# Optimization experiments

Measured on AMD Instinct MI355X. Metric: run time of the kernel, lower is better.

## Reference

```python
import jax, jax.numpy as jnp
import numpy as np

K_SIZE = 3
STRIDE = 1
DIL = 1
PAD = (K_SIZE - 1) // 2 * DIL          # padding of the deformable conv
OFF_PAD = (K_SIZE - 1) // 2            # padding of the offset conv
KK = K_SIZE * K_SIZE


def setup_inputs() -> dict:
    key = jax.random.key(0)
    k1, k2, k3, k4 = jax.random.split(key, 4)
    B, C, H, W = 4, 256, 64, 64
    O = 256
    x = jax.random.normal(k1, (B, C, H, W), jnp.float32)
    # offset/mask conv params (small so sampled offsets stay in a realistic range)
    w_off = jax.random.normal(k2, (3 * KK, C, K_SIZE, K_SIZE), jnp.float32) * 0.01
    b_off = jax.random.normal(k3, (3 * KK,), jnp.float32) * 0.01
    # deformable conv weight (conv_dcn has bias=False in the source)
    w_dcn = jax.random.normal(k4, (O, C, K_SIZE, K_SIZE), jnp.float32) * (1.0 / np.sqrt(C * KK))
    return {"x": x, "w_off": w_off, "b_off": b_off, "w_dcn": w_dcn}


def _bilinear_sample(x, ys, xs):
    """x: [B,C,H,W]; ys, xs: [B,KK,Ho,Wo] fractional coords. Zero outside bounds.
    Returns [B,C,KK,Ho,Wo]."""
    B, C, H, W = x.shape
    _, K, Ho, Wo = ys.shape
    y0 = jnp.floor(ys)
    x0 = jnp.floor(xs)
    y1, x1 = y0 + 1.0, x0 + 1.0
    wy1 = ys - y0
    wy0 = 1.0 - wy1
    wx1 = xs - x0
    wx0 = 1.0 - wx1
    x_flat = x.reshape(B, C, H * W)

    def gather_term(yi, xi, wt):
        valid = (yi >= 0) & (yi < H) & (xi >= 0) & (xi < W)
        yc = jnp.clip(yi, 0, H - 1).astype(jnp.int32)
        xc = jnp.clip(xi, 0, W - 1).astype(jnp.int32)
        idx = (yc * W + xc).reshape(B, -1)                      # [B, K*Ho*Wo]
        g = jax.vmap(lambda xf, i: xf[:, i])(x_flat, idx)       # [B, C, K*Ho*Wo]
        w = (wt * valid.astype(wt.dtype)).reshape(B, 1, -1)
        return g * w

    out = (gather_term(y0, x0, wy0 * wx0)
           + gather_term(y0, x1, wy0 * wx1)
           + gather_term(y1, x0, wy1 * wx0)
           + gather_term(y1, x1, wy1 * wx1))
    return out.reshape(B, C, K, Ho, Wo)


def _dcn_v2(x, w_off, b_off, w_dcn):
    B, C, H, W = x.shape
    # offset/mask conv (standard conv, padding (k-1)//2)
    om = jax.lax.conv_general_dilated(
        x, w_off, (STRIDE, STRIDE), [(OFF_PAD, OFF_PAD)] * 2,
        dimension_numbers=("NCHW", "OIHW", "NCHW")) + b_off[None, :, None, None]
    offset = om[:, :2 * KK]                 # [B, 2*KK, Ho, Wo] as (dy0,dx0,dy1,dx1,...)
    mask = jax.nn.sigmoid(om[:, 2 * KK:])   # [B, KK, Ho, Wo]
    Ho, Wo = offset.shape[2], offset.shape[3]

    off = offset.reshape(B, KK, 2, Ho, Wo)
    off_y, off_x = off[:, :, 0], off[:, :, 1]

    kh = (jnp.arange(KK) // K_SIZE).astype(jnp.float32)
    kw = (jnp.arange(KK) % K_SIZE).astype(jnp.float32)
    py = (jnp.arange(Ho) * STRIDE - PAD).astype(jnp.float32)
    px = (jnp.arange(Wo) * STRIDE - PAD).astype(jnp.float32)

    ys = py[None, None, :, None] + (kh * DIL)[None, :, None, None] + off_y
    xs = px[None, None, None, :] + (kw * DIL)[None, :, None, None] + off_x

    sampled = _bilinear_sample(x, ys, xs)           # [B,C,KK,Ho,Wo]
    sampled = sampled * mask[:, None]               # modulated (DCNv2)
    w = w_dcn.reshape(w_dcn.shape[0], C, KK)
    return jnp.einsum("bckhw,ock->bohw", sampled, w)


def reference(x, w_off, b_off, w_dcn):
    return _dcn_v2(x, w_off, b_off, w_dcn)
```

## Files before the change

kernel.cpp:

```cpp
#include <hip/hip_runtime.h>

typedef __attribute__((ext_vector_type(8))) short short8;
typedef __attribute__((ext_vector_type(4))) float f32x4;

#define CIN 256
#define OUTC 256
#define HWW 4096
#define IMG_H 64
#define IMG_W 64
#define SROW 264
#define SB __builtin_amdgcn_sched_barrier(0)
#define GLOAD(dst, addr) \
    asm volatile("global_load_dwordx4 %0, %1, off" : "=v"(dst) : "v"(addr) : "memory")
#define WAITVM(n) asm volatile("s_waitcnt vmcnt(" #n ")" ::: "memory")
#define WAITLGKM  asm volatile("s_waitcnt lgkmcnt(0)" ::: "memory")

__device__ __forceinline__ short f2bf(float f) {
    unsigned u = __float_as_uint(f);
    u += 0x7fffu + ((u >> 16) & 1u);
    return (short)(u >> 16);
}
__device__ __forceinline__ float bf2f(short s) {
    return __uint_as_float(((unsigned)(unsigned short)s) << 16);
}

__global__ __launch_bounds__(256) void prep(const float* __restrict__ x,
                                            const float* __restrict__ w_dcn,
                                            const float* __restrict__ w_off,
                                            short* __restrict__ xT,
                                            short* __restrict__ wF,
                                            short* __restrict__ wFo) {
    int bid = blockIdx.x;
    if (bid < 1024) {
        __shared__ float T[64][65];
        int p0 = (bid & 63) * 64;
        int c0 = ((bid >> 6) & 3) * 64;
        int b  = bid >> 8;
        int j = threadIdx.x & 63, i = threadIdx.x >> 6;
        const float* xb = x + ((size_t)b * CIN + c0) * HWW + p0;
#pragma unroll
        for (int k = 0; k < 16; ++k) {
            int row = i * 16 + k;
            T[row][j] = xb[(size_t)row * HWW + j];
        }
        __syncthreads();
        short* xTb = xT + ((size_t)b * HWW + p0) * CIN + c0;
#pragma unroll
        for (int k = 0; k < 16; ++k) {
            int prow = i * 16 + k;
            xTb[(size_t)prow * CIN + j] = f2bf(T[j][prow]);
        }
    } else if (bid < 1312) {
        int g = (bid - 1024) * 256 + threadIdx.x;
        int lane = g & 63;
        int rest = g >> 6;
        int octile = rest & 15;
        int step = rest >> 4;
        int kp = step >> 3, chv = step & 7;
        int oc = octile * 16 + (lane & 15);
        int cbase = chv * 32 + (lane >> 4) * 8;
        short8 v;
#pragma unroll
        for (int j = 0; j < 8; ++j)
            v[j] = f2bf(w_dcn[oc * 2304 + (cbase + j) * 9 + kp]);
        *(short8*)(wF + (size_t)g * 8) = v;
    } else {
        int g = (bid - 1312) * 256 + threadIdx.x;
        int lane = g & 63;
        int rest = g >> 6;
        int octile = rest & 1;
        int step = rest >> 1;
        int kp = step >> 3, chv = step & 7;
        int oc = octile * 16 + (lane & 15);
        int cbase = chv * 32 + (lane >> 4) * 8;
        short8 v;
#pragma unroll
        for (int j = 0; j < 8; ++j)
            v[j] = (oc < 27) ? f2bf(w_off[(oc * 256 + cbase + j) * 9 + kp]) : (short)0;
        *(short8*)(wFo + (size_t)g * 8) = v;
    }
}

__global__ __launch_bounds__(256) void offs_mfma(
        const short* __restrict__ xT, const short* __restrict__ wFo,
        float* __restrict__ P) {
    __shared__ short Sm[2][32 * SROW];

    int tid = threadIdx.x;
    int d = blockIdx.x;
    int L = (d & 7) * 64 + (d >> 3);
    int b = L >> 7;
    int ph = L & 127;
    int pbase = ph * 32;
    int prow = ph >> 1;
    int pc0 = (ph & 1) * 32;
    const short* xTb = xT + (size_t)b * HWW * CIN;

    int lane = tid & 63, wave = tid >> 6;
    int fr = lane & 15, fq = lane >> 4;
    int octile = wave & 1, pxt = wave >> 1;

    short8 st[4];

    auto loads = [&](int kp) {
        int yy = prow - 1 + kp / 3;
        int dx = kp % 3 - 1;
#pragma unroll
        for (int it = 0; it < 4; ++it) {
            int item = tid + it * 256;
            int cg8 = item & 31, px = item >> 5;
            int xx = pc0 + px + dx;
            bool ok = (yy >= 0 && yy < IMG_H && xx >= 0 && xx < IMG_W);
            int idx = ok ? ((yy * IMG_W + xx) * CIN + cg8 * 8) : 0;
            short8 v = *(const short8*)&xTb[idx];
            if (!ok) v = (short8){0,0,0,0,0,0,0,0};
            st[it] = v;
        }
    };
    auto writes = [&](int bufi) {
#pragma unroll
        for (int it = 0; it < 4; ++it) {
            int item = tid + it * 256;
            int cg8 = item & 31, px = item >> 5;
            *(short8*)&Sm[bufi][px * SROW + cg8 * 8] = st[it];
        }
    };

    f32x4 acc = (f32x4){0.f, 0.f, 0.f, 0.f};

    loads(0); writes(0);
    __syncthreads();
    for (int kp = 0; kp < 9; ++kp) {
        short8 aF[8];
#pragma unroll
        for (int chv = 0; chv < 8; ++chv)
            aF[chv] = *(const short8*)(wFo +
                    (((size_t)((kp * 8 + chv) * 2 + octile)) * 64 + lane) * 8);
        if (kp < 8) loads(kp + 1);
        const short* SmB = Sm[kp & 1];
#pragma unroll
        for (int chv = 0; chv < 8; ++chv) {
            short8 bF = *(const short8*)&SmB[(pxt * 16 + fr) * SROW + chv * 32 + fq * 8];
            acc = __builtin_amdgcn_mfma_f32_16x16x32_bf16(aF[chv], bF, acc, 0, 0, 0);
        }
        if (kp < 8) writes((kp + 1) & 1);
        __syncthreads();
    }

#pragma unroll
    for (int r = 0; r < 4; ++r) {
        int oc = octile * 16 + fq * 4 + r;
        if (oc < 27)
            P[((size_t)b * 32 + oc) * HWW + pbase + pxt * 16 + fr] = acc[r];
    }
}

__global__ __launch_bounds__(512, 2) void dcn_main(
        const short* __restrict__ xT, const float* __restrict__ b_off,
        const float* __restrict__ P, const short* __restrict__ wF,
        float* __restrict__ out) {
    __shared__ short Sm[2][16 * 64 * 8];
    __shared__ float4 preW[576];
    __shared__ int4  preI[576];

    int tid = threadIdx.x;
    int d = blockIdx.x;
    int L = (d & 7) * 32 + (d >> 3);
    int b = L >> 6;
    int row = L & 63;
    int pbase = row * 64;
    const short* xTb = xT + (size_t)b * HWW * CIN;

    for (int e = tid; e < 576; e += 512) {
        int px = e & 63, kp = e >> 6;
        int p = pbase + px;
        float oy = P[((size_t)b * 32 + 2 * kp) * HWW + p] + b_off[2 * kp];
        float ox = P[((size_t)b * 32 + 2 * kp + 1) * HWW + p] + b_off[2 * kp + 1];
        float ml = P[((size_t)b * 32 + 18 + kp) * HWW + p] + b_off[18 + kp];
        float m = 1.0f / (1.0f + expf(-ml));
        float ys = (float)(row - 1 + kp / 3) + oy;
        float xs = (float)(px - 1 + kp % 3) + ox;
        float y0f = floorf(ys), x0f = floorf(xs);
        float fy = ys - y0f, fx = xs - x0f;
        int iy0 = (int)y0f, ix0 = (int)x0f;
        int iy1 = iy0 + 1, ix1 = ix0 + 1;
        float vy0 = (iy0 >= 0 && iy0 < IMG_H) ? 1.f : 0.f;
        float vy1 = (iy1 >= 0 && iy1 < IMG_H) ? 1.f : 0.f;
        float vx0 = (ix0 >= 0 && ix0 < IMG_W) ? 1.f : 0.f;
        float vx1 = (ix1 >= 0 && ix1 < IMG_W) ? 1.f : 0.f;
        int ry0 = min(max(iy0, 0), IMG_H - 1) * IMG_W;
        int ry1 = min(max(iy1, 0), IMG_H - 1) * IMG_W;
        int cx0 = min(max(ix0, 0), IMG_W - 1);
        int cx1 = min(max(ix1, 0), IMG_W - 1);
        float wy0 = 1.f - fy, wy1 = fy, wx0 = 1.f - fx, wx1 = fx;
        preW[e] = make_float4(wy0 * wx0 * vy0 * vx0 * m, wy0 * wx1 * vy0 * vx1 * m,
                              wy1 * wx0 * vy1 * vx0 * m, wy1 * wx1 * vy1 * vx1 * m);
        preI[e] = make_int4((ry0 + cx0) * CIN, (ry0 + cx1) * CIN,
                            (ry1 + cx0) * CIN, (ry1 + cx1) * CIN);
    }
    __syncthreads();

    int lane = tid & 63, wave = tid >> 6;
    int fr = lane & 15, fq = lane >> 4;
    int chunk = tid & 15, p0 = tid >> 4;

    auto soff = [](int s, int px) { return (s * 64 + (px & 48) + ((px & 15) ^ s)) * 8; };

    short8 stO[2][8];
    short8 aFd[2][8];

    auto issue = [&](int t, int par) {
        int kp = t >> 1, ks = t & 1;
        int co = ks * 128 + chunk * 8;
#pragma unroll
        for (int cl = 0; cl < 4; ++cl)
#pragma unroll
            for (int m = 0; m < 2; ++m)
                GLOAD(aFd[par][cl * 2 + m], (const short8*)(wF +
                        (((size_t)((kp * 8 + ks * 4 + cl) * 16 + wave * 2 + m)) * 64 + lane) * 8));
#pragma unroll
        for (int it = 0; it < 2; ++it) {
            int px = p0 + it * 32;
            int4 iv = preI[kp * 64 + px];
            GLOAD(stO[par][it * 4 + 0], (const short8*)&xTb[iv.x + co]);
            GLOAD(stO[par][it * 4 + 1], (const short8*)&xTb[iv.y + co]);
            GLOAD(stO[par][it * 4 + 2], (const short8*)&xTb[iv.z + co]);
            GLOAD(stO[par][it * 4 + 3], (const short8*)&xTb[iv.w + co]);
        }
    };
    auto combine = [&](int t, int par) {
        int kp = t >> 1;
#pragma unroll
        for (int it = 0; it < 2; ++it) {
            int px = p0 + it * 32;
            float4 wv = preW[kp * 64 + px];
            short8 o;
#pragma unroll
            for (int j = 0; j < 8; ++j) {
                float v = wv.x * bf2f(stO[par][it * 4 + 0][j]) +
                          wv.y * bf2f(stO[par][it * 4 + 1][j]) +
                          wv.z * bf2f(stO[par][it * 4 + 2][j]) +
                          wv.w * bf2f(stO[par][it * 4 + 3][j]);
                o[j] = f2bf(v);
            }
            *(short8*)&Sm[par][soff(chunk, px)] = o;
        }
    };

    f32x4 acc[2][4];
#pragma unroll
    for (int m = 0; m < 2; ++m)
#pragma unroll
        for (int n = 0; n < 4; ++n)
            acc[m][n] = (f32x4){0.f, 0.f, 0.f, 0.f};

    issue(0, 0);
    SB;

#pragma unroll
    for (int t = 0; t < 18; ++t) {
        const int par = t & 1;
        if (t < 17) issue(t + 1, par ^ 1);
        SB;
        if (t < 17) { WAITVM(16); } else { WAITVM(0); }
        SB;
        combine(t, par);
        SB;
        WAITLGKM;
        __builtin_amdgcn_s_barrier();
        SB;
        {
            const short* SmB = Sm[par];
#pragma unroll
            for (int cl = 0; cl < 4; ++cl)
#pragma unroll
                for (int n = 0; n < 4; ++n) {
                    short8 bF = *(const short8*)&SmB[soff(cl * 4 + fq, n * 16 + fr)];
#pragma unroll
                    for (int m = 0; m < 2; ++m)
                        acc[m][n] = __builtin_amdgcn_mfma_f32_16x16x32_bf16(
                                aFd[par][cl * 2 + m], bF, acc[m][n], 0, 0, 0);
                }
        }
        SB;
    }

    float* outb = out + (size_t)b * (OUTC * HWW) + pbase;
#pragma unroll
    for (int m = 0; m < 2; ++m)
#pragma unroll
        for (int n = 0; n < 4; ++n)
#pragma unroll
            for (int r = 0; r < 4; ++r)
                outb[(size_t)(wave * 32 + m * 16 + fq * 4 + r) * HWW + n * 16 + fr] =
                        acc[m][n][r];
}

extern "C" void kernel_launch(void* const* d_in, const int* in_sizes, int n_in,
                              void* d_out, int out_size, void* d_ws, size_t ws_size,
                              hipStream_t stream) {
    const float* x     = (const float*)d_in[0];
    const float* w_off = (const float*)d_in[1];
    const float* b_off = (const float*)d_in[2];
    const float* w_dcn = (const float*)d_in[3];
    float* out = (float*)d_out;

    short* xT  = (short*)d_ws;
    float* P   = (float*)(xT + (size_t)4 * HWW * CIN);
    short* wF  = (short*)(P + (size_t)4 * 32 * HWW);
    short* wFo = wF + (size_t)73728 * 8;

    prep<<<1348, 256, 0, stream>>>(x, w_dcn, w_off, xT, wF, wFo);
    offs_mfma<<<512, 256, 0, stream>>>(xT, wFo, P);
    dcn_main<<<256, 512, 0, stream>>>(xT, b_off, P, wF, out);
}
```

Before: 60.99 us.

## Warp-specialize DCN main loop into MFMA consumer and gather producer waves

Splits the block's waves into two roles. Waves 0-3 load the weight fragments and run the MFMA accumulation over a 64-row output slice each. Waves 4+ gather the bilinear taps, combine them into bf16 and write the sampled tile to LDS one stage ahead. Gather latency and combine arithmetic are meant to overlap with the matrix work instead of running in lockstep, at the cost of more registers per wave (larger accumulators and buffers) and a barrier handshake whose counts must match across roles. It also assumes the launch provides at least 8 waves, which is not visible here.

```diff
diff --git a/kernel.cpp b/kernel.cpp
--- a/kernel.cpp
+++ b/kernel.cpp
@@ -201,99 +201,126 @@
     __syncthreads();
 
     int lane = tid & 63, wave = tid >> 6;
-    int fr = lane & 15, fq = lane >> 4;
-    int chunk = tid & 15, p0 = tid >> 4;
-
     auto soff = [](int s, int px) { return (s * 64 + (px & 48) + ((px & 15) ^ s)) * 8; };
 
-    short8 stO[2][8];
-    short8 aFd[2][8];
-
-    auto issue = [&](int t, int par) {
-        int kp = t >> 1, ks = t & 1;
-        int co = ks * 128 + chunk * 8;
-#pragma unroll
-        for (int cl = 0; cl < 4; ++cl)
-#pragma unroll
-            for (int m = 0; m < 2; ++m)
-                GLOAD(aFd[par][cl * 2 + m], (const short8*)(wF +
-                        (((size_t)((kp * 8 + ks * 4 + cl) * 16 + wave * 2 + m)) * 64 + lane) * 8));
-#pragma unroll
-        for (int it = 0; it < 2; ++it) {
-            int px = p0 + it * 32;
-            int4 iv = preI[kp * 64 + px];
-            GLOAD(stO[par][it * 4 + 0], (const short8*)&xTb[iv.x + co]);
-            GLOAD(stO[par][it * 4 + 1], (const short8*)&xTb[iv.y + co]);
-            GLOAD(stO[par][it * 4 + 2], (const short8*)&xTb[iv.z + co]);
-            GLOAD(stO[par][it * 4 + 3], (const short8*)&xTb[iv.w + co]);
-        }
-    };
-    auto combine = [&](int t, int par) {
-        int kp = t >> 1;
-#pragma unroll
-        for (int it = 0; it < 2; ++it) {
-            int px = p0 + it * 32;
-            float4 wv = preW[kp * 64 + px];
-            short8 o;
-#pragma unroll
-            for (int j = 0; j < 8; ++j) {
-                float v = wv.x * bf2f(stO[par][it * 4 + 0][j]) +
-                          wv.y * bf2f(stO[par][it * 4 + 1][j]) +
-                          wv.z * bf2f(stO[par][it * 4 + 2][j]) +
-                          wv.w * bf2f(stO[par][it * 4 + 3][j]);
-                o[j] = f2bf(v);
+    if (wave < 4) {
+        int fr = lane & 15, fq = lane >> 4;
+        short8 aA[16], aB[16];
+
+        auto issue_aF = [&](int t, short8* buf) {
+            int kp = t >> 1, ks = t & 1;
+#pragma unroll
+            for (int cl = 0; cl < 4; ++cl)
+#pragma unroll
+                for (int m = 0; m < 4; ++m)
+                    GLOAD(buf[cl * 4 + m], (const short8*)(wF +
+                            (((size_t)((kp * 8 + ks * 4 + cl) * 16 + wave * 4 + m)) * 64 + lane) * 8));
+        };
+
+        f32x4 acc[4][4];
+#pragma unroll
+        for (int m = 0; m < 4; ++m)
+#pragma unroll
+            for (int n = 0; n < 4; ++n)
+                acc[m][n] = (f32x4){0.f, 0.f, 0.f, 0.f};
+
+        issue_aF(0, aA);
+        SB;
+        __builtin_amdgcn_s_barrier();
+
+#pragma unroll
+        for (int t = 0; t < 18; ++t) {
+            short8* cur = (t & 1) ? aB : aA;
+            short8* nxt = (t & 1) ? aA : aB;
+            if (t < 17) issue_aF(t + 1, nxt);
+            SB;
+            if (t < 17) { WAITVM(16); } else { WAITVM(0); }
+            SB;
+            const short* SmB = Sm[t & 1];
+#pragma unroll
+            for (int cl = 0; cl < 4; ++cl)
+#pragma unroll
+                for (int n = 0; n < 4; ++n) {
+                    short8 bF = *(const short8*)&SmB[soff(cl * 4 + fq, n * 16 + fr)];
+#pragma unroll
+                    for (int m = 0; m < 4; ++m)
+                        acc[m][n] = __builtin_amdgcn_mfma_f32_16x16x32_bf16(
+                                cur[cl * 4 + m], bF, acc[m][n], 0, 0, 0);
+                }
+            SB;
+            __builtin_amdgcn_s_barrier();
+        }
+
+        float* outb = out + (size_t)b * (OUTC * HWW) + pbase;
+#pragma unroll
+        for (int m = 0; m < 4; ++m)
+#pragma unroll
+            for (int n = 0; n < 4; ++n)
+#pragma unroll
+                for (int r = 0; r < 4; ++r)
+                    outb[(size_t)(wave * 64 + m * 16 + fq * 4 + r) * HWW + n * 16 + fr] =
+                            acc[m][n][r];
+    } else {
+        int ptid = tid - 256;
+        int chunk = ptid & 15, p0 = ptid >> 4;
+        short8 sA[16], sB[16];
+
+        auto issue_taps = [&](int t, short8* buf) {
+            int kp = t >> 1, ks = t & 1;
+            int co = ks * 128 + chunk * 8;
+#pragma unroll
+            for (int it = 0; it < 4; ++it) {
+                int px = p0 + it * 16;
+                int4 iv = preI[kp * 64 + px];
+                GLOAD(buf[it * 4 + 0], (const short8*)&xTb[iv.x + co]);
+                GLOAD(buf[it * 4 + 1], (const short8*)&xTb[iv.y + co]);
+                GLOAD(buf[it * 4 + 2], (const short8*)&xTb[iv.z + co]);
+                GLOAD(buf[it * 4 + 3], (const short8*)&xTb[iv.w + co]);
             }
-            *(short8*)&Sm[par][soff(chunk, px)] = o;
-        }
-    };
-
-    f32x4 acc[2][4];
-#pragma unroll
-    for (int m = 0; m < 2; ++m)
-#pragma unroll
-        for (int n = 0; n < 4; ++n)
-            acc[m][n] = (f32x4){0.f, 0.f, 0.f, 0.f};
-
-    issue(0, 0);
-    SB;
-
-#pragma unroll
-    for (int t = 0; t < 18; ++t) {
-        const int par = t & 1;
-        if (t < 17) issue(t + 1, par ^ 1);
+        };
+        auto combine = [&](int t, short8* buf) {
+            int kp = t >> 1;
+            short* SmW = Sm[t & 1];
+#pragma unroll
+            for (int it = 0; it < 4; ++it) {
+                int px = p0 + it * 16;
+                float4 wv = preW[kp * 64 + px];
+                short8 o;
+#pragma unroll
+                for (int j = 0; j < 8; ++j) {
+                    float v = wv.x * bf2f(buf[it * 4 + 0][j]) +
+                              wv.y * bf2f(buf[it * 4 + 1][j]) +
+                              wv.z * bf2f(buf[it * 4 + 2][j]) +
+                              wv.w * bf2f(buf[it * 4 + 3][j]);
+                    o[j] = f2bf(v);
+                }
+                *(short8*)&SmW[soff(chunk, px)] = o;
+            }
+        };
+
+        issue_taps(0, sA);
+        issue_taps(1, sB);
         SB;
-        if (t < 17) { WAITVM(16); } else { WAITVM(0); }
+        WAITVM(16);
         SB;
-        combine(t, par);
-        SB;
+        combine(0, sA);
         WAITLGKM;
         __builtin_amdgcn_s_barrier();
-        SB;
-        {
-            const short* SmB = Sm[par];
-#pragma unroll
-            for (int cl = 0; cl < 4; ++cl)
-#pragma unroll
-                for (int n = 0; n < 4; ++n) {
-                    short8 bF = *(const short8*)&SmB[soff(cl * 4 + fq, n * 16 + fr)];
-#pragma unroll
-                    for (int m = 0; m < 2; ++m)
-                        acc[m][n] = __builtin_amdgcn_mfma_f32_16x16x32_bf16(
-                                aFd[par][cl * 2 + m], bF, acc[m][n], 0, 0, 0);
-                }
-        }
-        SB;
-    }
-
-    float* outb = out + (size_t)b * (OUTC * HWW) + pbase;
-#pragma unroll
-    for (int m = 0; m < 2; ++m)
-#pragma unroll
-        for (int n = 0; n < 4; ++n)
-#pragma unroll
-            for (int r = 0; r < 4; ++r)
-                outb[(size_t)(wave * 32 + m * 16 + fq * 4 + r) * HWW + n * 16 + fr] =
-                        acc[m][n][r];
+
+#pragma unroll
+        for (int t = 0; t < 17; ++t) {
+            short8* cur = (t & 1) ? sA : sB;
+            short8* nxt = (t & 1) ? sB : sA;
+            if (t < 16) issue_taps(t + 2, nxt);
+            SB;
+            if (t < 16) { WAITVM(16); } else { WAITVM(0); }
+            SB;
+            combine(t + 1, cur);
+            WAITLGKM;
+            __builtin_amdgcn_s_barrier();
+        }
+        __builtin_amdgcn_s_barrier();
+    }
 }
 
 extern "C" void kernel_launch(void* const* d_in, const int* in_sizes, int n_in,
```

After: 62.75 us. 2.9% more time.
